# Kernel optimization log

Hardware: AMD Instinct MI355X
Metric: run time of the kernel (lower is better)

## Reference

```python
import jax, jax.numpy as jnp
import numpy as np

K = 3
OFFSET_SCALE = 0.25
GN_GROUPS = 8
GN_EPS = 1e-5


def setup_inputs() -> dict:
    key = jax.random.key(0)
    k1, k2, k3 = jax.random.split(key, 3)
    N, C, H, W = 4, 128, 96, 96
    Cout = 128
    x = jax.random.normal(k1, (N, C, H, W), dtype=jnp.float32)
    # offset head: small random weights so offsets are modest (tanh tames anyway)
    w_head = jax.random.normal(k2, (3, C, 3, 3), dtype=jnp.float32) * 0.05
    b_head = jnp.zeros((3,), dtype=jnp.float32)
    # kaiming-ish scale for the deform conv weight: sqrt(2 / fan_out)
    w_dcn = jax.random.normal(k3, (Cout, C, 3, 3), dtype=jnp.float32) * np.sqrt(2.0 / (Cout * 9))
    gn_gamma = jnp.ones((Cout,), dtype=jnp.float32)
    gn_beta = jnp.zeros((Cout,), dtype=jnp.float32)
    return {"x": x, "w_head": w_head, "b_head": b_head, "w_dcn": w_dcn,
            "gn_gamma": gn_gamma, "gn_beta": gn_beta}


def _conv3x3(x, w, b):
    y = jax.lax.conv_general_dilated(
        x, w, window_strides=(1, 1), padding=((1, 1), (1, 1)),
        dimension_numbers=("NCHW", "OIHW", "NCHW"))
    return y + b[None, :, None, None]


def _deform_sample(xn, py, px):
    # xn: (C,H,W); py/px: (9,H,W) absolute sampling coords (y=row, x=col)
    C, H, W = xn.shape
    y0 = jnp.floor(py).astype(jnp.int32)
    x0 = jnp.floor(px).astype(jnp.int32)
    fy = py - y0
    fx = px - x0
    xf = xn.reshape(C, H * W)

    def corner(yi, xi, wgt):
        valid = (yi >= 0) & (yi < H) & (xi >= 0) & (xi < W)
        idx = jnp.clip(yi, 0, H - 1) * W + jnp.clip(xi, 0, W - 1)  # (9,H,W)
        v = xf[:, idx.reshape(-1)].reshape(C, *idx.shape)  # (C,9,H,W)
        return v * (wgt * valid)[None]

    return (corner(y0, x0, (1 - fy) * (1 - fx))
            + corner(y0, x0 + 1, (1 - fy) * fx)
            + corner(y0 + 1, x0, fy * (1 - fx))
            + corner(y0 + 1, x0 + 1, fy * fx))


def reference(x, w_head, b_head, w_dcn, gn_gamma, gn_beta):
    N, C, H, W = x.shape
    Cout = w_dcn.shape[0]
    stride, pad, dil = 1, 1, 1

    head = _conv3x3(x, w_head, b_head)                 # (N,3,H,W)
    dx, dy, m = head[:, :1], head[:, 1:2], head[:, 2:3]
    mask = jax.nn.sigmoid(m)                           # (N,1,H,W) broadcast over 9 taps
    dx = OFFSET_SCALE * jnp.tanh(dx)
    dy = OFFSET_SCALE * jnp.tanh(dy)

    # serpentine 18-channel offsets, mmcv layout: (oy, ox) pairs per kernel tap
    z = jnp.zeros_like(dx)
    offs = jnp.concatenate(
        [z, z, z, dy, z, -dy, dx, z, z, z, -dx, z, dx, dy, dx, -dy, -dx, dy], axis=1)
    offs = offs.reshape(N, 9, 2, H, W)
    oy, ox = offs[:, :, 0], offs[:, :, 1]              # (N,9,H,W)

    ky = jnp.arange(9) // 3
    kx = jnp.arange(9) % 3
    base_y = (jnp.arange(H) * stride - pad)[None, :, None] + (ky * dil)[:, None, None]
    base_x = (jnp.arange(W) * stride - pad)[None, None, :] + (kx * dil)[:, None, None]
    py = base_y[None] + oy                             # (N,9,H,W)
    px = base_x[None] + ox

    sampled = jax.vmap(_deform_sample)(x, py, px)      # (N,C,9,H,W)
    sampled = sampled * mask[:, None]                  # modulated

    y = jnp.einsum('nckhw,ock->nohw', sampled, w_dcn.reshape(Cout, C, 9))

    # GroupNorm(8, Cout) + ReLU
    G = min(GN_GROUPS, Cout)
    yg = y.reshape(N, G, Cout // G, H, W)
    mu = yg.mean(axis=(2, 3, 4), keepdims=True)
    var = yg.var(axis=(2, 3, 4), keepdims=True)
    yn = ((yg - mu) * jax.lax.rsqrt(var + GN_EPS)).reshape(N, Cout, H, W)
    yn = yn * gn_gamma[None, :, None, None] + gn_beta[None, :, None, None]
    return jax.nn.relu(yn)
```

## Files before the change

kernel.cpp:

```cpp
#include <hip/hip_runtime.h>
#include <hip/hip_bf16.h>
#include <math.h>

#define NB   4
#define CIN  128
#define HH   96
#define WW   96
#define HWN  (HH*WW)
#define NHW  (NB*HWN)
#define COUT 128
#define KW   9
#define KDIM (CIN*KW)
#define GSZ  16
#define PXB  32
#define NBLK (NHW/PXB)
#define XPB  64
#define XPOB (NHW/XPB)

typedef __attribute__((ext_vector_type(8))) short bf16x8;
typedef __attribute__((ext_vector_type(4))) float f32x4;

#define OFF_WAH   0
#define OFF_DX    147456
#define OFF_DY    184320
#define OFF_MASK  221184
#define OFF_GN    258048
#define OFF_MAP   258240
#define OFF_PAIR  258496
#define OFF_XT    258560

#define HEADB 1152

__device__ __forceinline__ ushort f2bf(float f) {
    union { float f; uint u; } v; v.f = f;
    uint r = v.u + 0x7fffu + ((v.u >> 16) & 1u);
    return (ushort)(r >> 16);
}

__device__ __forceinline__ void barrier_keep_vm() {
    asm volatile("s_waitcnt lgkmcnt(0)\n\ts_barrier" ::: "memory");
}

__global__ __launch_bounds__(256) void pre_kernel(const float* __restrict__ x,
                                                  const float* __restrict__ w_head,
                                                  const float* __restrict__ b_head,
                                                  const float* __restrict__ wd,
                                                  ushort* __restrict__ wah,
                                                  float* __restrict__ dxv,
                                                  float* __restrict__ dyv,
                                                  float* __restrict__ maskv,
                                                  float* __restrict__ gn_part,
                                                  int* __restrict__ map,
                                                  int* __restrict__ pairB,
                                                  float* __restrict__ xt) {
    __shared__ __attribute__((aligned(16))) float smem[8480];
    const int b = blockIdx.x, t = threadIdx.x;

    if (b >= HEADB + 576) {
        float (*tile)[XPB + 1] = (float (*)[XPB + 1])smem;
        int* sperm = (int*)(smem + CIN * (XPB + 1));
        int* spair = (int*)(smem + CIN * (XPB + 1) + CIN);
        const int bb2 = b - (HEADB + 576);
        const int p0 = bb2 * XPB;
        const int n  = p0 / HWN, hw0 = p0 % HWN;
        const float* xn = x + (size_t)n * CIN * HWN + hw0;

        if (t < 64) {
            int l = t;
            union { bf16x8 v; short a[8]; } B;
#pragma unroll
            for (int e = 0; e < 8; ++e) {
                float val = (float)(1u << (((l >> 4) * 8 + e) & 31));
                B.a[e] = (short)f2bf(val);
            }
#pragma unroll
            for (int s = 0; s < 32; ++s) {
                union { bf16x8 v; short a[8]; } A;
#pragma unroll
                for (int e = 0; e < 8; ++e) A.a[e] = 0;
                if ((l >> 4) == (s >> 3)) A.a[s & 7] = (short)f2bf(1.0f);
                f32x4 d = {0.f, 0.f, 0.f, 0.f};
                d = __builtin_amdgcn_mfma_f32_16x16x32_bf16(A.v, B.v, d, 0, 0, 0);
                float v0 = d[0];
                if (l == 0 && v0 > 0.f) {
                    int ex; frexpf(v0, &ex);
                    int j = ex - 1;
                    if (j >= 0 && j < 32) spair[j] = s;
                }
            }
        }
        __syncthreads();
        if (t < CIN) sperm[t] = (t & ~31) | (spair[t & 31] & 31);
        __syncthreads();

#pragma unroll
        for (int rep = 0; rep < 4; ++rep) {
            const int c  = rep * 32 + (t >> 3);
            const int px = (t & 7) * 8;
            const float* src = xn + (size_t)c * HWN + px;
            float4 a = *(const float4*)src;
            float4 bq = *(const float4*)(src + 4);
            tile[c][px + 0] = a.x;  tile[c][px + 1] = a.y;
            tile[c][px + 2] = a.z;  tile[c][px + 3] = a.w;
            tile[c][px + 4] = bq.x; tile[c][px + 5] = bq.y;
            tile[c][px + 6] = bq.z; tile[c][px + 7] = bq.w;
        }
        __syncthreads();

#pragma unroll
        for (int wc = 0; wc < 8; ++wc) {
            const int idx = wc * 256 + t;
            const int px  = idx >> 5;
            const int s4  = idx & 31;
            float4 v;
            v.x = tile[sperm[s4 * 4 + 0]][px];
            v.y = tile[sperm[s4 * 4 + 1]][px];
            v.z = tile[sperm[s4 * 4 + 2]][px];
            v.w = tile[sperm[s4 * 4 + 3]][px];
            *(float4*)(xt + ((size_t)(p0 + px)) * CIN + s4 * 4) = v;
        }
        return;
    }

    if (b >= HEADB) {
        const int bb = b - HEADB;
        int i = bb * 256 + t;
        {
            int e  = i & 7;
            int l  = (i >> 3) & 63;
            int ot = (i >> 9) & 7;
            int q  = (i >> 12) & 3;
            int k  = i >> 14;
            int o  = ot * 16 + (l & 15);
            int c  = q * 32 + (l >> 4) * 8 + e;
            wah[i] = f2bf(wd[o * KDIM + c * KW + k]);
        }
        if (bb == 0 && t < 128) gn_part[t] = 0.f;
        if (bb == 0 && t < 64) {
            int l = t;
            bf16x8 A1 = {}, B1 = {}, A2 = {}, B2 = {};
            if ((l >> 4) == 0) {
                A1[0] = (short)f2bf((float)((l & 15) + 1));
                B1[0] = (short)f2bf(1.0f);
                A2[0] = (short)f2bf(1.0f);
                B2[0] = (short)f2bf((float)((l & 15) + 1));
            }
            f32x4 d1 = {0.f,0.f,0.f,0.f}, d2 = {0.f,0.f,0.f,0.f};
            d1 = __builtin_amdgcn_mfma_f32_16x16x32_bf16(A1, B1, d1, 0, 0, 0);
            d2 = __builtin_amdgcn_mfma_f32_16x16x32_bf16(A2, B2, d2, 0, 0, 0);
#pragma unroll
            for (int r = 0; r < 4; ++r) {
                int m = (int)(d1[r] + 0.5f) - 1;
                int n = (int)(d2[r] + 0.5f) - 1;
                map[l * 4 + r] = (m << 4) | n;
            }
        }
        if (bb == 1 && t < 64) {
            int l = t;
            union { bf16x8 v; short a[8]; } B;
#pragma unroll
            for (int e = 0; e < 8; ++e) {
                float val = (float)(1u << (((l >> 4) * 8 + e) & 31));
                B.a[e] = (short)f2bf(val);
            }
#pragma unroll
            for (int s = 0; s < 32; ++s) {
                union { bf16x8 v; short a[8]; } A;
#pragma unroll
                for (int e = 0; e < 8; ++e) A.a[e] = 0;
                if ((l >> 4) == (s >> 3)) A.a[s & 7] = (short)f2bf(1.0f);
                f32x4 d = {0.f, 0.f, 0.f, 0.f};
                d = __builtin_amdgcn_mfma_f32_16x16x32_bf16(A.v, B.v, d, 0, 0, 0);
                float v0 = d[0];
                if (l == 0 && v0 > 0.f) {
                    int ex; frexpf(v0, &ex);
                    int j = ex - 1;
                    if (j >= 0 && j < 32) pairB[j] = s;
                }
            }
        }
        return;
    }

    float* wl = smem;
    float (*sp)[8][13] = (float (*)[8][13])(smem + CIN * 28);
    for (int i = t; i < 3456; i += 256) {
        int j = i / KDIM, r = i - j * KDIM;
        int c = r / 9, kk = r - c * 9;
        wl[c * 28 + kk * 3 + j] = w_head[i];
    }
    __syncthreads();

    const int sl = t & 7;
    const int cg = t >> 3;
    const int p0 = b * 32 + sl * 4;
    const int n  = p0 / HWN;
    const int hw = p0 - n * HWN;
    const int h  = hw / WW;
    const int w0 = hw - h * WW;
    const float* xn = x + (size_t)n * CIN * HWN;
    const bool lok = (w0 > 0);
    const bool rok = (w0 < WW - 4);

    float acc[12];
#pragma unroll
    for (int i = 0; i < 12; ++i) acc[i] = 0.f;

#pragma unroll
    for (int cc = 0; cc < 4; ++cc) {
        const int c = cg * 4 + cc;
        const float* xc = xn + (size_t)c * HWN;
        float v[3][6];
#pragma unroll
        for (int r = 0; r < 3; ++r) {
            int y = h - 1 + r;
            if (y >= 0 && y < HH) {
                const float* xr = xc + y * WW + w0;
                float4 m4 = *(const float4*)xr;
                v[r][1] = m4.x; v[r][2] = m4.y; v[r][3] = m4.z; v[r][4] = m4.w;
                v[r][0] = lok ? xr[-1] : 0.f;
                v[r][5] = rok ? xr[4]  : 0.f;
            } else {
#pragma unroll
                for (int i = 0; i < 6; ++i) v[r][i] = 0.f;
            }
        }
        float wr[28];
        const float* wc = &wl[c * 28];
#pragma unroll
        for (int i2 = 0; i2 < 7; ++i2) {
            float4 q4 = *(const float4*)(wc + i2 * 4);
            wr[i2 * 4 + 0] = q4.x; wr[i2 * 4 + 1] = q4.y;
            wr[i2 * 4 + 2] = q4.z; wr[i2 * 4 + 3] = q4.w;
        }
#pragma unroll
        for (int ky = 0; ky < 3; ++ky)
#pragma unroll
            for (int kx = 0; kx < 3; ++kx) {
                const int kk = ky * 3 + kx;
                const float wj0 = wr[kk * 3 + 0];
                const float wj1 = wr[kk * 3 + 1];
                const float wj2 = wr[kk * 3 + 2];
#pragma unroll
                for (int q = 0; q < 4; ++q) {
                    float val = v[ky][q + kx];
                    acc[q * 3 + 0] = fmaf(val, wj0, acc[q * 3 + 0]);
                    acc[q * 3 + 1] = fmaf(val, wj1, acc[q * 3 + 1]);
                    acc[q * 3 + 2] = fmaf(val, wj2, acc[q * 3 + 2]);
                }
            }
    }
#pragma unroll
    for (int i = 0; i < 12; ++i) sp[cg][sl][i] = acc[i];
    __syncthreads();
    if (cg < 8) {
#pragma unroll
        for (int k = 8; k < 32; k += 8)
#pragma unroll
            for (int i = 0; i < 12; ++i) sp[cg][sl][i] += sp[cg + k][sl][i];
    }
    __syncthreads();
    if (t < 32) {
        const int s2 = t >> 2, q = t & 3;
        float b0 = b_head[0], b1 = b_head[1], b2 = b_head[2];
#pragma unroll
        for (int cgi = 0; cgi < 8; ++cgi) {
            b0 += sp[cgi][s2][q * 3 + 0];
            b1 += sp[cgi][s2][q * 3 + 1];
            b2 += sp[cgi][s2][q * 3 + 2];
        }
        int pp = b * 32 + t;
        dxv[pp]   = 0.25f * tanhf(b0);
        dyv[pp]   = 0.25f * tanhf(b1);
        maskv[pp] = 1.f / (1.f + expf(-b2));
    }
}

__global__ __launch_bounds__(256) void dcn_kernel(const float* __restrict__ xt,
                                                  const ushort* __restrict__ wah,
                                                  const float* __restrict__ dxv,
                                                  const float* __restrict__ dyv,
                                                  const float* __restrict__ maskv,
                                                  const int* __restrict__ map,
                                                  float* __restrict__ out,
                                                  float* __restrict__ gn_part) {
    __shared__ __attribute__((aligned(16))) ushort sBh[2][4 * PXB * 8];
    __shared__ float sMask[PXB];
    __shared__ float gred[16];

    const int t = threadIdx.x;
    const int lane = t & 63;
    const int wv = t >> 6;
    const int lg = lane >> 4;
    const int ml = lane & 15;
    const int pix = t >> 3;
    const int sg  = t & 7;

    int b = blockIdx.x;
    int nb = (b & 7) * (NBLK / 8) + (b >> 3);
    const int p0  = nb * PXB;
    const int n   = p0 / HWN;
    const int hw0 = p0 % HWN;
    const float* xtn = xt + (size_t)n * HWN * CIN;

    if (t < PXB) sMask[t] = maskv[p0 + t];
    if (t < 16) gred[t] = 0.f;

    const float dxl = dxv[p0 + pix];
    const float dyl = dyv[p0 + pix];
    const int hme = (hw0 + pix) / WW;
    const int wme = (hw0 + pix) % WW;

    f32x4 acc[2][2];
#pragma unroll
    for (int i = 0; i < 2; i++)
#pragma unroll
        for (int j = 0; j < 2; j++) acc[i][j] = (f32x4){0.f, 0.f, 0.f, 0.f};

    const int oyc[9] = {0, 0, 0, 1, 0, -1, 1, 1, -1};
    const int oxc[9] = {0, 1, -1, 0, 0, 0, 1, -1, 1};
    const int ncl[9] = {1, 2, 2, 2, 1, 2, 4, 4, 4};

    int aa[4]; float wq[4];
    float4 vr0, vr1, vr2, vr3;
    bf16x8 An0, An1;

    {
        float py = (float)(hme - 1), px = (float)(wme - 1);
        float fy0 = floorf(py), fx0 = floorf(px);
        int y0 = (int)fy0, x0 = (int)fx0;
        float fy = py - fy0, fx = px - fx0;
#pragma unroll
        for (int j = 0; j < 4; ++j) {
            int yy = y0 + (j >> 1), xx = x0 + (j & 1);
            float wb = ((j >> 1) ? fy : 1.f - fy) * ((j & 1) ? fx : 1.f - fx);
            bool ok = (yy >= 0) && (yy < HH) && (xx >= 0) && (xx < WW);
            aa[j] = min(max(yy, 0), HH - 1) * WW + min(max(xx, 0), WW - 1);
            wq[j] = ok ? wb : 0.f;
        }
        vr0 = *(const float4*)(xtn + ((aa[0] << 7) + sg * 4));
        const size_t abase = (size_t)(wv * 2) * 512 + lane * 8;
        An0 = *(const bf16x8*)(wah + abase);
        An1 = *(const bf16x8*)(wah + abase + 512);
    }

#pragma unroll
    for (int j = 0; j < 36; ++j) {
        const int k = j >> 2;
        const int NC = ncl[k];
        bf16x8 Ah0 = An0, Ah1 = An1;
        union { short4 v; ushort u[4]; } hv;
        {
            float s0 = vr0.x * wq[0], s1 = vr0.y * wq[0];
            float s2 = vr0.z * wq[0], s3 = vr0.w * wq[0];
            if (NC >= 2) {
                s0 = fmaf(vr1.x, wq[1], s0); s1 = fmaf(vr1.y, wq[1], s1);
                s2 = fmaf(vr1.z, wq[1], s2); s3 = fmaf(vr1.w, wq[1], s3);
            }
            if (NC == 4) {
                s0 = fmaf(vr2.x, wq[2], s0); s1 = fmaf(vr2.y, wq[2], s1);
                s2 = fmaf(vr2.z, wq[2], s2); s3 = fmaf(vr2.w, wq[2], s3);
                s0 = fmaf(vr3.x, wq[3], s0); s1 = fmaf(vr3.y, wq[3], s1);
                s2 = fmaf(vr3.z, wq[3], s2); s3 = fmaf(vr3.w, wq[3], s3);
            }
            hv.u[0] = f2bf(s0); hv.u[1] = f2bf(s1);
            hv.u[2] = f2bf(s2); hv.u[3] = f2bf(s3);
        }
        const int wbase = ((sg >> 1) * PXB + pix) * 8 + (sg & 1) * 4;
        *(short4*)&sBh[j & 1][wbase] = hv.v;
        if (j < 35) {
            const int jn = j + 1, kn = jn >> 2, qn = jn & 3;
            if (qn == 0) {
                const int ky = kn / 3, kx = kn - ky * 3;
                float py = (float)(hme - 1 + ky) + (float)oyc[kn] * dxl;
                float px = (float)(wme - 1 + kx) + (float)oxc[kn] * dyl;
                float fy0 = floorf(py), fx0 = floorf(px);
                int y0 = (int)fy0, x0 = (int)fx0;
                float fy = py - fy0, fx = px - fx0;
#pragma unroll
                for (int jj = 0; jj < 4; ++jj) {
                    int yy = y0 + (jj >> 1), xx = x0 + (jj & 1);
                    float wb = ((jj >> 1) ? fy : 1.f - fy) * ((jj & 1) ? fx : 1.f - fx);
                    bool ok = (yy >= 0) && (yy < HH) && (xx >= 0) && (xx < WW);
                    aa[jj] = min(max(yy, 0), HH - 1) * WW + min(max(xx, 0), WW - 1);
                    wq[jj] = ok ? wb : 0.f;
                }
                if (ncl[kn] == 2 && oxc[kn] == 0) { aa[1] = aa[2]; wq[1] = wq[2]; }
            }
            const int NCn = ncl[kn];
            const int co = qn * 32 + sg * 4;
            vr0 = *(const float4*)(xtn + ((aa[0] << 7) + co));
            if (NCn >= 2) vr1 = *(const float4*)(xtn + ((aa[1] << 7) + co));
            if (NCn == 4) {
                vr2 = *(const float4*)(xtn + ((aa[2] << 7) + co));
                vr3 = *(const float4*)(xtn + ((aa[3] << 7) + co));
            }
            const size_t abase = (size_t)((kn * 4 + qn) * 8 + wv * 2) * 512 + lane * 8;
            An0 = *(const bf16x8*)(wah + abase);
            An1 = *(const bf16x8*)(wah + abase + 512);
        }
        barrier_keep_vm();
#pragma unroll
        for (int pt = 0; pt < 2; ++pt) {
            const int rbase = (lg * PXB + pt * 16 + ml) * 8;
            bf16x8 Bh = *(const bf16x8*)&sBh[j & 1][rbase];
            acc[0][pt] = __builtin_amdgcn_mfma_f32_16x16x32_bf16(Ah0, Bh, acc[0][pt], 0, 0, 0);
            acc[1][pt] = __builtin_amdgcn_mfma_f32_16x16x32_bf16(Ah1, Bh, acc[1][pt], 0, 0, 0);
        }
    }

    int4 mn4 = *(const int4*)&map[lane * 4];
    int mn[4] = {mn4.x, mn4.y, mn4.z, mn4.w};
    float s1g[2] = {0.f, 0.f}, s2g[2] = {0.f, 0.f};
#pragma unroll
    for (int ot = 0; ot < 2; ++ot) {
        int otile = wv * 32 + ot * 16;
#pragma unroll
        for (int pt = 0; pt < 2; ++pt) {
#pragma unroll
            for (int r = 0; r < 4; ++r) {
                int m = mn[r] >> 4, nn2 = mn[r] & 15;
                int p = pt * 16 + nn2;
                float v = acc[ot][pt][r] * sMask[p];
                s1g[ot] += v;
                s2g[ot] += v * v;
                out[((size_t)n * COUT + otile + m) * HWN + hw0 + p] = v;
            }
        }
    }
#pragma unroll
    for (int ot = 0; ot < 2; ++ot) {
        int g = wv * 2 + ot;
        atomicAdd(&gred[g * 2 + 0], s1g[ot]);
        atomicAdd(&gred[g * 2 + 1], s2g[ot]);
    }
    __syncthreads();
    if (t < 8) {
        atomicAdd(&gn_part[n * 8 + t],      gred[t * 2 + 0]);
        atomicAdd(&gn_part[64 + n * 8 + t], gred[t * 2 + 1]);
    }
}

__global__ __launch_bounds__(256) void gn_apply(float* __restrict__ out,
                                                const float* __restrict__ gn_part,
                                                const float* __restrict__ gamma,
                                                const float* __restrict__ beta) {
    int i4 = blockIdx.x * 256 + threadIdx.x;
    size_t e = (size_t)i4 * 4;
    int og = (int)(e / HWN);
    int n = og >> 7, o = og & 127;
    int s = n * 8 + (o >> 4);
    const float cnt = (float)GSZ * (float)HWN;
    float s1 = gn_part[s], s2 = gn_part[64 + s];
    float mu = s1 / cnt;
    float var = s2 / cnt - mu * mu;
    float inv = rsqrtf(var + 1e-5f);
    float ga = gamma[o] * inv;
    float be = beta[o] - mu * ga;
    float4 v = *(float4*)(out + e);
    v.x = fmaxf(fmaf(v.x, ga, be), 0.f);
    v.y = fmaxf(fmaf(v.y, ga, be), 0.f);
    v.z = fmaxf(fmaf(v.z, ga, be), 0.f);
    v.w = fmaxf(fmaf(v.w, ga, be), 0.f);
    *(float4*)(out + e) = v;
}

extern "C" void kernel_launch(void* const* d_in, const int* in_sizes, int n_in,
                              void* d_out, int out_size, void* d_ws, size_t ws_size,
                              hipStream_t stream) {
    const float* x       = (const float*)d_in[0];
    const float* w_head  = (const float*)d_in[1];
    const float* b_head  = (const float*)d_in[2];
    const float* w_dcn   = (const float*)d_in[3];
    const float* gamma   = (const float*)d_in[4];
    const float* beta    = (const float*)d_in[5];
    float* out = (float*)d_out;
    float* ws  = (float*)d_ws;

    ushort* wah    = (ushort*)(ws + OFF_WAH);
    float* dxv     = ws + OFF_DX;
    float* dyv     = ws + OFF_DY;
    float* maskv   = ws + OFF_MASK;
    float* gn_part = ws + OFF_GN;
    int*   map     = (int*)(ws + OFF_MAP);
    int*   pairB   = (int*)(ws + OFF_PAIR);
    float* xt      = ws + OFF_XT;

    pre_kernel<<<HEADB + 576 + XPOB, 256, 0, stream>>>(x, w_head, b_head, w_dcn, wah,
                                                       dxv, dyv, maskv, gn_part, map, pairB, xt);
    dcn_kernel<<<NBLK, 256, 0, stream>>>(xt, wah, dxv, dyv, maskv, map, out, gn_part);
    gn_apply<<<(NB * COUT * HWN) / 4 / 256, 256, 0, stream>>>(out, gn_part, gamma, beta);
}
```

Measured before the change: 159.6 us.

## Deepen gather prefetch to two steps ahead in deformable conv main loop

```diff
diff --git a/kernel.cpp b/kernel.cpp
--- a/kernel.cpp
+++ b/kernel.cpp
@@ -276,7 +276,7 @@
     }
 }
 
-__global__ __launch_bounds__(256) void dcn_kernel(const float* __restrict__ xt,
+__global__ __launch_bounds__(256, 3) void dcn_kernel(const float* __restrict__ xt,
                                                   const ushort* __restrict__ wah,
                                                   const float* __restrict__ dxv,
                                                   const float* __restrict__ dyv,
@@ -321,93 +321,90 @@
     const int oxc[9] = {0, 1, -1, 0, 0, 0, 1, -1, 1};
     const int ncl[9] = {1, 2, 2, 2, 1, 2, 4, 4, 4};
 
-    int aa[4]; float wq[4];
-    float4 vr0, vr1, vr2, vr3;
-    bf16x8 An0, An1;
-
-    {
-        float py = (float)(hme - 1), px = (float)(wme - 1);
-        float fy0 = floorf(py), fx0 = floorf(px);
-        int y0 = (int)fy0, x0 = (int)fx0;
-        float fy = py - fy0, fx = px - fx0;
-#pragma unroll
-        for (int j = 0; j < 4; ++j) {
-            int yy = y0 + (j >> 1), xx = x0 + (j & 1);
-            float wb = ((j >> 1) ? fy : 1.f - fy) * ((j & 1) ? fx : 1.f - fx);
-            bool ok = (yy >= 0) && (yy < HH) && (xx >= 0) && (xx < WW);
-            aa[j] = min(max(yy, 0), HH - 1) * WW + min(max(xx, 0), WW - 1);
-            wq[j] = ok ? wb : 0.f;
-        }
-        vr0 = *(const float4*)(xtn + ((aa[0] << 7) + sg * 4));
-        const size_t abase = (size_t)(wv * 2) * 512 + lane * 8;
-        An0 = *(const bf16x8*)(wah + abase);
-        An1 = *(const bf16x8*)(wah + abase + 512);
-    }
+    int    aa[2][4];
+    float  wq[2][4];
+    float4 vr[2][4];
+    bf16x8 An[2][2];
+
+#define CORNERS(kn_, cs_) {                                                    \
+    const int ky = (kn_) / 3, kx = (kn_) - ky * 3;                             \
+    float py = (float)(hme - 1 + ky) + (float)oyc[kn_] * dxl;                  \
+    float px = (float)(wme - 1 + kx) + (float)oxc[kn_] * dyl;                  \
+    float fy0 = floorf(py), fx0 = floorf(px);                                  \
+    int y0 = (int)fy0, x0 = (int)fx0;                                          \
+    float fy = py - fy0, fx = px - fx0;                                        \
+    _Pragma("unroll")                                                          \
+    for (int jj = 0; jj < 4; ++jj) {                                           \
+        int yy = y0 + (jj >> 1), xx = x0 + (jj & 1);                           \
+        float wb = ((jj >> 1) ? fy : 1.f - fy) * ((jj & 1) ? fx : 1.f - fx);   \
+        bool ok = (yy >= 0) && (yy < HH) && (xx >= 0) && (xx < WW);            \
+        aa[cs_][jj] = min(max(yy, 0), HH - 1) * WW + min(max(xx, 0), WW - 1);  \
+        wq[cs_][jj] = ok ? wb : 0.f;                                           \
+    }                                                                          \
+    if (ncl[kn_] == 2 && oxc[kn_] == 0) {                                      \
+        aa[cs_][1] = aa[cs_][2]; wq[cs_][1] = wq[cs_][2];                      \
+    } }
+
+#define ISSUE(jn_, rs_, cs_) {                                                 \
+    const int qn_ = (jn_) & 3, NCn_ = ncl[(jn_) >> 2];                         \
+    const int co_ = qn_ * 32 + sg * 4;                                         \
+    vr[rs_][0] = *(const float4*)(xtn + ((aa[cs_][0] << 7) + co_));            \
+    if (NCn_ >= 2) vr[rs_][1] = *(const float4*)(xtn + ((aa[cs_][1] << 7) + co_)); \
+    if (NCn_ == 4) {                                                           \
+        vr[rs_][2] = *(const float4*)(xtn + ((aa[cs_][2] << 7) + co_));        \
+        vr[rs_][3] = *(const float4*)(xtn + ((aa[cs_][3] << 7) + co_));        \
+    }                                                                          \
+    const size_t abase_ = (size_t)((jn_) * 8 + wv * 2) * 512 + lane * 8;       \
+    An[rs_][0] = *(const bf16x8*)(wah + abase_);                               \
+    An[rs_][1] = *(const bf16x8*)(wah + abase_ + 512);                         \
+    }
+
+    CORNERS(0, 0);
+    ISSUE(0, 0, 0);
+    ISSUE(1, 1, 0);
 
 #pragma unroll
     for (int j = 0; j < 36; ++j) {
-        const int k = j >> 2;
+        const int k  = j >> 2;
         const int NC = ncl[k];
-        bf16x8 Ah0 = An0, Ah1 = An1;
+        const int cs = k & 1;
+        const int rs = j & 1;
+        bf16x8 Ah0 = An[rs][0], Ah1 = An[rs][1];
         union { short4 v; ushort u[4]; } hv;
         {
-            float s0 = vr0.x * wq[0], s1 = vr0.y * wq[0];
-            float s2 = vr0.z * wq[0], s3 = vr0.w * wq[0];
+            float s0 = vr[rs][0].x * wq[cs][0], s1 = vr[rs][0].y * wq[cs][0];
+            float s2 = vr[rs][0].z * wq[cs][0], s3 = vr[rs][0].w * wq[cs][0];
             if (NC >= 2) {
-                s0 = fmaf(vr1.x, wq[1], s0); s1 = fmaf(vr1.y, wq[1], s1);
-                s2 = fmaf(vr1.z, wq[1], s2); s3 = fmaf(vr1.w, wq[1], s3);
+                s0 = fmaf(vr[rs][1].x, wq[cs][1], s0); s1 = fmaf(vr[rs][1].y, wq[cs][1], s1);
+                s2 = fmaf(vr[rs][1].z, wq[cs][1], s2); s3 = fmaf(vr[rs][1].w, wq[cs][1], s3);
             }
             if (NC == 4) {
-                s0 = fmaf(vr2.x, wq[2], s0); s1 = fmaf(vr2.y, wq[2], s1);
-                s2 = fmaf(vr2.z, wq[2], s2); s3 = fmaf(vr2.w, wq[2], s3);
-                s0 = fmaf(vr3.x, wq[3], s0); s1 = fmaf(vr3.y, wq[3], s1);
-                s2 = fmaf(vr3.z, wq[3], s2); s3 = fmaf(vr3.w, wq[3], s3);
+                s0 = fmaf(vr[rs][2].x, wq[cs][2], s0); s1 = fmaf(vr[rs][2].y, wq[cs][2], s1);
+                s2 = fmaf(vr[rs][2].z, wq[cs][2], s2); s3 = fmaf(vr[rs][2].w, wq[cs][2], s3);
+                s0 = fmaf(vr[rs][3].x, wq[cs][3], s0); s1 = fmaf(vr[rs][3].y, wq[cs][3], s1);
+                s2 = fmaf(vr[rs][3].z, wq[cs][3], s2); s3 = fmaf(vr[rs][3].w, wq[cs][3], s3);
             }
             hv.u[0] = f2bf(s0); hv.u[1] = f2bf(s1);
             hv.u[2] = f2bf(s2); hv.u[3] = f2bf(s3);
         }
         const int wbase = ((sg >> 1) * PXB + pix) * 8 + (sg & 1) * 4;
-        *(short4*)&sBh[j & 1][wbase] = hv.v;
-        if (j < 35) {
-            const int jn = j + 1, kn = jn >> 2, qn = jn & 3;
-            if (qn == 0) {
-                const int ky = kn / 3, kx = kn - ky * 3;
-                float py = (float)(hme - 1 + ky) + (float)oyc[kn] * dxl;
-                float px = (float)(wme - 1 + kx) + (float)oxc[kn] * dyl;
-                float fy0 = floorf(py), fx0 = floorf(px);
-                int y0 = (int)fy0, x0 = (int)fx0;
-                float fy = py - fy0, fx = px - fx0;
-#pragma unroll
-                for (int jj = 0; jj < 4; ++jj) {
-                    int yy = y0 + (jj >> 1), xx = x0 + (jj & 1);
-                    float wb = ((jj >> 1) ? fy : 1.f - fy) * ((jj & 1) ? fx : 1.f - fx);
-                    bool ok = (yy >= 0) && (yy < HH) && (xx >= 0) && (xx < WW);
-                    aa[jj] = min(max(yy, 0), HH - 1) * WW + min(max(xx, 0), WW - 1);
-                    wq[jj] = ok ? wb : 0.f;
-                }
-                if (ncl[kn] == 2 && oxc[kn] == 0) { aa[1] = aa[2]; wq[1] = wq[2]; }
-            }
-            const int NCn = ncl[kn];
-            const int co = qn * 32 + sg * 4;
-            vr0 = *(const float4*)(xtn + ((aa[0] << 7) + co));
-            if (NCn >= 2) vr1 = *(const float4*)(xtn + ((aa[1] << 7) + co));
-            if (NCn == 4) {
-                vr2 = *(const float4*)(xtn + ((aa[2] << 7) + co));
-                vr3 = *(const float4*)(xtn + ((aa[3] << 7) + co));
-            }
-            const size_t abase = (size_t)((kn * 4 + qn) * 8 + wv * 2) * 512 + lane * 8;
-            An0 = *(const bf16x8*)(wah + abase);
-            An1 = *(const bf16x8*)(wah + abase + 512);
+        *(short4*)&sBh[rs][wbase] = hv.v;
+        if (j < 34) {
+            const int jn = j + 2, kn = jn >> 2, qn = jn & 3, csn = kn & 1;
+            if (qn == 0) CORNERS(kn, csn);
+            ISSUE(jn, rs, csn);
         }
         barrier_keep_vm();
 #pragma unroll
         for (int pt = 0; pt < 2; ++pt) {
             const int rbase = (lg * PXB + pt * 16 + ml) * 8;
-            bf16x8 Bh = *(const bf16x8*)&sBh[j & 1][rbase];
+            bf16x8 Bh = *(const bf16x8*)&sBh[rs][rbase];
             acc[0][pt] = __builtin_amdgcn_mfma_f32_16x16x32_bf16(Ah0, Bh, acc[0][pt], 0, 0, 0);
             acc[1][pt] = __builtin_amdgcn_mfma_f32_16x16x32_bf16(Ah1, Bh, acc[1][pt], 0, 0, 0);
         }
     }
+#undef CORNERS
+#undef ISSUE
 
     int4 mn4 = *(const int4*)&map[lane * 4];
     int mn[4] = {mn4.x, mn4.y, mn4.z, mn4.w};
```

Result: no change. 157.9 us (-1.1%).
